# Kernel tuning notes

Hardware: AMD Instinct MI355X
Metric: run time of the kernel (lower is better)

## Reference

```python
import jax, jax.numpy as jnp
import numpy as np

NUM_EMBEDDINGS = 2048
EMBEDDING_DIM = 256
COMMITMENT_COST = 0.25


def setup_inputs() -> dict:
    key = jax.random.key(0)
    k1, k2 = jax.random.split(key)
    z_e = jax.random.normal(k1, (64, EMBEDDING_DIM, 32, 32), dtype=jnp.float32)
    # nn.Embedding weight initialized uniform(-1/K, 1/K)
    bound = 1.0 / NUM_EMBEDDINGS
    codebook = jax.random.uniform(k2, (NUM_EMBEDDINGS, EMBEDDING_DIM),
                                  dtype=jnp.float32, minval=-bound, maxval=bound)
    return {"z_e": z_e, "codebook": codebook}


def reference(z_e, codebook):
    B, C, H, W = z_e.shape  # C == embedding_dim
    K = codebook.shape[0]
    sg = jax.lax.stop_gradient

    # [B, C, H, W] -> [B*H*W, C]
    z_e_flat = jnp.transpose(z_e, (0, 2, 3, 1)).reshape(-1, C)

    # squared L2 distances: ||z||^2 - 2 z E^T + ||E||^2  -> [N, K]
    distances = (jnp.sum(z_e_flat ** 2, axis=1, keepdims=True)
                 - 2.0 * jnp.matmul(z_e_flat, codebook.T)
                 + jnp.sum(codebook ** 2, axis=1))
    indices = jnp.argmin(distances, axis=1)  # [N]

    encodings = jax.nn.one_hot(indices, K, dtype=z_e_flat.dtype)  # [N, K]
    z_q_flat = codebook[indices]  # [N, C] embedding gather
    z_q = jnp.transpose(z_q_flat.reshape(B, H, W, C), (0, 3, 1, 2))

    codebook_loss = jnp.mean((z_q_flat - sg(z_e_flat)) ** 2)
    commitment_loss = jnp.mean((sg(z_q_flat) - z_e_flat) ** 2)
    loss = codebook_loss + COMMITMENT_COST * commitment_loss

    e_mean = jnp.mean(encodings, axis=0)  # [K]
    perplexity = jnp.exp(-jnp.sum(e_mean * jnp.log(e_mean + 1e-10)))

    # straight-through estimator
    z_q_st = z_e + sg(z_q - z_e)
    return z_q_st, loss, perplexity, encodings
```

## Files before the change

### kernel.cpp

```cpp
#include <hip/hip_runtime.h>
#include <hip/hip_bf16.h>
#include <math.h>

#define NTOT 65536
#define KCB  2048
#define CDIM 256
#define HW   1024

#define OUT_LOSS 16777216
#define OUT_PERP 16777217
#define OUT_ENC  16777218

#define ZB_OFF_F  16777232
#define CBB_OFF_F 33554448

#define WS_SROW 0
#define WS_CK   262144
#define WS_IDX  270336
#define WS_CNT  532480
#define WS_PART 540672

#define MARGIN 3e-3f
#define CAP 4096

typedef __attribute__((ext_vector_type(8))) short short8;
typedef __attribute__((ext_vector_type(4))) float f32x4;

__device__ inline unsigned enc_f(float x) {
    unsigned u = __float_as_uint(x);
    return (u & 0x80000000u) ? ~u : (u | 0x80000000u);
}
__device__ inline float dec_f(unsigned e) {
    unsigned u = (e & 0x80000000u) ? (e ^ 0x80000000u) : ~e;
    return __uint_as_float(u);
}

__device__ inline void lds_min_u64(unsigned long long* p, unsigned long long v) {
    unsigned long long old = *p;
    while (v < old) {
        unsigned long long assumed = old;
        old = atomicCAS(p, assumed, v);
        if (old == assumed) break;
    }
}

__global__ __launch_bounds__(256) void k_prep_cb(const float* __restrict__ cb, ushort* __restrict__ cbb,
                                                 float* __restrict__ ck, int* __restrict__ cntK) {
    int wv = threadIdx.x >> 6, lane = threadIdx.x & 63;
    int r = blockIdx.x * 4 + wv;
    const float* row = cb + (size_t)r * CDIM;
    float4 v = *(const float4*)(row + lane * 4);
    ushort4 o;
    __hip_bfloat16 h;
    h = __float2bfloat16(v.x); o.x = *(ushort*)&h;
    h = __float2bfloat16(v.y); o.y = *(ushort*)&h;
    h = __float2bfloat16(v.z); o.z = *(ushort*)&h;
    h = __float2bfloat16(v.w); o.w = *(ushort*)&h;
    *(ushort4*)(cbb + (size_t)r * CDIM + lane * 4) = o;
    float s = v.x*v.x + v.y*v.y + v.z*v.z + v.w*v.w;
    for (int off = 32; off >= 1; off >>= 1) s += __shfl_down(s, off, 64);
    if (lane == 0) ck[r] = s;
    if (lane == 1) cntK[r] = 0;
}

__global__ __launch_bounds__(256) void k_rownorm(const float* __restrict__ z, float* __restrict__ srow) {
    int n = blockIdx.x * 256 + threadIdx.x;
    int b = n >> 10, hw = n & 1023;
    const float* base = z + (size_t)b * (CDIM * HW) + hw;
    float s = 0.f;
#pragma unroll 8
    for (int c = 0; c < CDIM; ++c) { float v = base[(size_t)c * HW]; s = fmaf(v, v, s); }
    srow[n] = s;
}

__global__ __launch_bounds__(256) void k_prep_z(const float* __restrict__ z, ushort* __restrict__ zb) {
    __shared__ float tile[64][65];
    int tid = threadIdx.x;
    int bid = blockIdx.x;
    int hwT = bid & 15, cT = (bid >> 4) & 3, b = bid >> 6;
    int c0 = cT * 64, hw0 = hwT * 64;
    int w = tid >> 6, hw = tid & 63;
#pragma unroll
    for (int l = 0; l < 16; ++l) {
        int c = l * 4 + w;
        tile[c][hw] = z[((size_t)b * CDIM + (c0 + c)) * HW + hw0 + hw];
    }
    __syncthreads();
    int r = tid >> 2, g = tid & 3;
    union { ushort u[16]; int4 v[2]; } pk;
#pragma unroll
    for (int j = 0; j < 16; ++j) {
        __hip_bfloat16 h = __float2bfloat16(tile[g * 16 + j][r]);
        pk.u[j] = *(ushort*)&h;
    }
    size_t n = (size_t)b * HW + hw0 + r;
    ushort* dst = zb + n * CDIM + c0 + g * 16;
    *(int4*)(dst) = pk.v[0];
    *(int4*)(dst + 8) = pk.v[1];
}

__global__ __launch_bounds__(256, 2) void k_mfma_argmin(
    const ushort* __restrict__ zb, const ushort* __restrict__ cbb,
    const float* __restrict__ z, const float* __restrict__ cb,
    const float* __restrict__ srow, const float* __restrict__ ckg,
    int* __restrict__ indices, int* __restrict__ cntK)
{
    __shared__ unsigned rowminU[64];
    __shared__ int   candRK[CAP];
    __shared__ float candD[CAP];
    __shared__ int   cnt;
    __shared__ float thrF[64];
    __shared__ unsigned long long best[64];

    const int tid = threadIdx.x;
    const int w = tid >> 6, lane = tid & 63;
    const int col = lane & 15, quad = lane >> 4;
    const int n0 = blockIdx.x * 64;

    short8 areg[4][8];
#pragma unroll
    for (int nt = 0; nt < 4; ++nt)
#pragma unroll
        for (int cs = 0; cs < 8; ++cs)
            areg[nt][cs] = *(const short8*)(zb + ((size_t)(n0 + nt * 16 + col)) * CDIM + cs * 32 + quad * 8);

    if (tid < 64) { rowminU[tid] = 0xFFFFFFFFu; best[tid] = ~0ull; }
    if (tid == 0) cnt = 0;

    float gmin[16];
#pragma unroll
    for (int s = 0; s < 16; ++s) gmin[s] = INFINITY;
    __syncthreads();

    int npass = 1;
    for (int pass = 0; pass < npass; ++pass) {
        for (int k0 = 0; k0 < KCB; k0 += 128) {
            const int kb = k0 + w * 32;
            f32x4 acc[4][2];
#pragma unroll
            for (int nt = 0; nt < 4; ++nt)
#pragma unroll
                for (int kt = 0; kt < 2; ++kt)
                    acc[nt][kt] = (f32x4){0.f, 0.f, 0.f, 0.f};
#pragma unroll
            for (int kt = 0; kt < 2; ++kt) {
                short8 bfrag[8];
#pragma unroll
                for (int cs = 0; cs < 8; ++cs)
                    bfrag[cs] = *(const short8*)(cbb + ((size_t)(kb + kt * 16 + col)) * CDIM + cs * 32 + quad * 8);
#pragma unroll
                for (int nt = 0; nt < 4; ++nt)
#pragma unroll
                    for (int cs = 0; cs < 8; ++cs)
                        acc[nt][kt] = __builtin_amdgcn_mfma_f32_16x16x32_bf16(areg[nt][cs], bfrag[cs], acc[nt][kt], 0, 0, 0);
            }
            if (pass == 0) {
#pragma unroll
                for (int kt = 0; kt < 2; ++kt) {
                    const float ckv = ckg[kb + kt * 16 + col];
#pragma unroll
                    for (int nt = 0; nt < 4; ++nt)
#pragma unroll
                        for (int r = 0; r < 4; ++r) {
                            float dt = fmaf(-2.0f, acc[nt][kt][r], ckv);
                            const int s = nt * 4 + r;
                            if (dt < gmin[s]) {
                                gmin[s] = dt;
                                atomicMin(&rowminU[nt * 16 + quad * 4 + r], enc_f(dt));
                            }
                        }
                }
            }
            __syncthreads();
#pragma unroll
            for (int s = 0; s < 16; ++s) {
                int row = (s >> 2) * 16 + quad * 4 + (s & 3);
                gmin[s] = fminf(gmin[s], dec_f(rowminU[row]));
            }
#pragma unroll
            for (int kt = 0; kt < 2; ++kt) {
                const int k = kb + kt * 16 + col;
                const float ckv = ckg[k];
#pragma unroll
                for (int nt = 0; nt < 4; ++nt)
#pragma unroll
                    for (int r = 0; r < 4; ++r) {
                        float dt = fmaf(-2.0f, acc[nt][kt][r], ckv);
                        const int s = nt * 4 + r;
                        if (dt <= gmin[s] + MARGIN) {
                            int p = atomicAdd(&cnt, 1);
                            if (p < CAP) {
                                candRK[p] = ((nt * 16 + quad * 4 + r) << 16) | k;
                                candD[p] = dt;
                            }
                        }
                    }
            }
        }
        __syncthreads();
        if (pass == 0 && cnt > CAP) {
            npass = 2;
            if (tid == 0) cnt = 0;
            __syncthreads();
        }
    }
    const int nc = min(cnt, CAP);
    if (tid < 64) thrF[tid] = dec_f(rowminU[tid]) + MARGIN;
    __syncthreads();

    const int b = n0 >> 10, hw0 = n0 & 1023;
    for (int t = tid; t < nc; t += 256) {
        const int rc = candRK[t];
        const int row = rc >> 16, k = rc & 0xFFFF;
        if (candD[t] > thrF[row]) continue;
        const float* zp = z + (size_t)b * (CDIM * HW) + hw0 + row;
        const float* cp = cb + (size_t)k * CDIM;
        float m = 0.f;
#pragma unroll 8
        for (int c = 0; c < CDIM; ++c) m = fmaf(zp[(size_t)c << 10], cp[c], m);
        float d = (srow[n0 + row] - 2.0f * m) + ckg[k];
        unsigned long long pk = ((unsigned long long)__float_as_uint(d) << 32) | (unsigned)k;
        lds_min_u64(&best[row], pk);
    }
    __syncthreads();
    if (tid < 64) {
        int bk = (int)(best[tid] & 0xFFFFFFFFull);
        indices[n0 + tid] = bk;
        atomicAdd(&cntK[bk], 1);
    }
}

__global__ __launch_bounds__(256, 2) void k_gather(const float* __restrict__ z, const float* __restrict__ cb,
                                                   const int* __restrict__ idx, float* __restrict__ out0,
                                                   double* __restrict__ part) {
    __shared__ float qt[CDIM * 64];
    __shared__ double sh[256];
    const int tid = threadIdx.x;
    const int nl = tid & 63, cg = tid >> 6;
    const int n0 = blockIdx.x * 64;
    const int b = n0 >> 10, hw0 = n0 & 1023;
    const int k = idx[n0 + nl];
    const float* crow = cb + (size_t)k * CDIM + cg * 64;
#pragma unroll
    for (int j4 = 0; j4 < 16; ++j4) {
        float4 v = *(const float4*)(crow + j4 * 4);
        int c = cg * 64 + j4 * 4;
        qt[(c + 0) * 64 + nl] = v.x;
        qt[(c + 1) * 64 + nl] = v.y;
        qt[(c + 2) * 64 + nl] = v.z;
        qt[(c + 3) * 64 + nl] = v.w;
    }
    __syncthreads();
    double acc = 0.0;
    const size_t ebase = ((size_t)b * CDIM) * HW + hw0 + nl;
#pragma unroll 4
    for (int j = 0; j < 64; ++j) {
        int c = cg * 64 + j;
        size_t e = ebase + ((size_t)c << 10);
        float ze = z[e];
        float q = qt[c * 64 + nl];
        float d = q - ze;
        out0[e] = ze + d;
        acc += (double)d * (double)d;
    }
    sh[tid] = acc;
    __syncthreads();
    for (int s = 128; s > 0; s >>= 1) {
        if (tid < s) sh[tid] += sh[tid + s];
        __syncthreads();
    }
    if (tid == 0) part[blockIdx.x] = sh[0];
}

__global__ __launch_bounds__(256) void k_encodings(const int* __restrict__ idx, float4* __restrict__ p4,
                                                   float* __restrict__ tail) {
    __shared__ int sidx[17];
    const int tid = threadIdx.x;
    const size_t g0 = (size_t)blockIdx.x * 8192;
    const long f0 = 4L * (long)g0 - 2;
    int nlo = (int)(f0 >> 11); if (nlo < 0) nlo = 0;
    if (tid < 17) { int n = nlo + tid; sidx[tid] = (n < NTOT) ? idx[n] : -1; }
    __syncthreads();
    const float4 zv = make_float4(0.f, 0.f, 0.f, 0.f);
    for (int i = 0; i < 32; ++i) {
        size_t g = g0 + (size_t)i * 256 + tid;
        long fe = 4L * (long)g - 2;
        float4 v = zv;
        if (fe < 0) {
            int kk = sidx[0];
            if (kk == 0) v.z = 1.f;
            if (kk == 1) v.w = 1.f;
        } else {
            int n = (int)(fe >> 11);
            int k0c = (int)(fe & 2047);
            if (k0c >= 2045) {
#pragma unroll
                for (int j = 0; j < 4; ++j) {
                    long fej = fe + j;
                    int nj = (int)(fej >> 11);
                    int kj = (int)(fej & 2047);
                    int li = nj - nlo;
                    int kk = (li >= 0 && li < 17) ? sidx[li] : -2;
                    ((float*)&v)[j] = (kk == kj) ? 1.f : 0.f;
                }
            } else {
                int d = sidx[n - nlo] - k0c;
                if (d >= 0 && d < 4) ((float*)&v)[d] = 1.f;
            }
        }
        p4[g] = v;
    }
    if (blockIdx.x == 0 && tid == 0) {
        int kk = idx[NTOT - 1];
        tail[0] = (kk == 2046) ? 1.f : 0.f;
        tail[1] = (kk == 2047) ? 1.f : 0.f;
    }
}

__global__ __launch_bounds__(256) void k_finalize(const double* __restrict__ part, const int* __restrict__ cnt,
                                                  float* __restrict__ out) {
    __shared__ double sh[256];
    double a = 0.0;
    for (int i = threadIdx.x; i < 1024; i += 256) a += part[i];
    sh[threadIdx.x] = a; __syncthreads();
    for (int s = 128; s > 0; s >>= 1) { if (threadIdx.x < s) sh[threadIdx.x] += sh[threadIdx.x + s]; __syncthreads(); }
    double total = sh[0];
    __syncthreads();
    double p = 0.0;
    for (int i = threadIdx.x; i < 2048; i += 256) {
        double pm = (double)cnt[i] / 65536.0;
        p += pm * log(pm + 1e-10);
    }
    sh[threadIdx.x] = p; __syncthreads();
    for (int s = 128; s > 0; s >>= 1) { if (threadIdx.x < s) sh[threadIdx.x] += sh[threadIdx.x + s]; __syncthreads(); }
    if (threadIdx.x == 0) {
        double mean = total / ((double)NTOT * (double)CDIM);
        out[OUT_LOSS] = (float)(mean * 1.25);
        out[OUT_PERP] = (float)exp(-sh[0]);
    }
}

extern "C" void kernel_launch(void* const* d_in, const int* in_sizes, int n_in,
                              void* d_out, int out_size, void* d_ws, size_t ws_size,
                              hipStream_t stream) {
    const float* z  = (const float*)d_in[0];
    const float* cb = (const float*)d_in[1];
    float* out = (float*)d_out;
    char* ws = (char*)d_ws;
    float*  srow = (float*)(ws + WS_SROW);
    float*  ck   = (float*)(ws + WS_CK);
    int*    idx  = (int*)(ws + WS_IDX);
    int*    cnt  = (int*)(ws + WS_CNT);
    double* part = (double*)(ws + WS_PART);
    ushort* zb  = (ushort*)(out + ZB_OFF_F);
    ushort* cbb = (ushort*)(out + CBB_OFF_F);

    hipLaunchKernelGGL(k_prep_cb,     dim3(512),  dim3(256), 0, stream, cb, cbb, ck, cnt);
    hipLaunchKernelGGL(k_rownorm,     dim3(256),  dim3(256), 0, stream, z, srow);
    hipLaunchKernelGGL(k_prep_z,      dim3(4096), dim3(256), 0, stream, z, zb);
    hipLaunchKernelGGL(k_mfma_argmin, dim3(1024), dim3(256), 0, stream, zb, cbb, z, cb, srow, ck, idx, cnt);
    hipLaunchKernelGGL(k_gather,      dim3(1024), dim3(256), 0, stream, z, cb, idx, out, part);
    hipLaunchKernelGGL(k_encodings,   dim3(4096), dim3(256), 0, stream, idx, (float4*)(out + OUT_LOSS),
                       out + (OUT_LOSS + (size_t)33554432 * 4));
    hipLaunchKernelGGL(k_finalize,    dim3(1),    dim3(256), 0, stream, part, cnt, out);
}
```

Measured before the change: 1.004 ms.

## Fuse prep kernels and restructure argmin with warm-start min and per-wave candidate lists

Merges the three preprocessing kernels into one launch with block-range dispatch. The argmin kernel now seeds the row minima from one codebook tile, then runs a single pass that updates minima and collects candidates together, with no per-tile block barrier. Candidates go into per-wave LDS lists of row/index only, so the candidate-distance array is gone. LDS drops enough to raise launch bounds to 3 blocks per CU. The trade-off is a looser candidate threshold early in the scan, which can mean more exact-refinement work, plus a full fallback rescan if any wave list overflows.

```diff
diff --git a/kernel.cpp b/kernel.cpp
--- a/kernel.cpp
+++ b/kernel.cpp
@@ -21,7 +21,7 @@
 #define WS_PART 540672
 
 #define MARGIN 3e-3f
-#define CAP 4096
+#define WCAP 1024
 
 typedef __attribute__((ext_vector_type(8))) short short8;
 typedef __attribute__((ext_vector_type(4))) float f32x4;
@@ -44,72 +44,92 @@
     }
 }
 
-__global__ __launch_bounds__(256) void k_prep_cb(const float* __restrict__ cb, ushort* __restrict__ cbb,
-                                                 float* __restrict__ ck, int* __restrict__ cntK) {
-    int wv = threadIdx.x >> 6, lane = threadIdx.x & 63;
-    int r = blockIdx.x * 4 + wv;
-    const float* row = cb + (size_t)r * CDIM;
-    float4 v = *(const float4*)(row + lane * 4);
-    ushort4 o;
-    __hip_bfloat16 h;
-    h = __float2bfloat16(v.x); o.x = *(ushort*)&h;
-    h = __float2bfloat16(v.y); o.y = *(ushort*)&h;
-    h = __float2bfloat16(v.z); o.z = *(ushort*)&h;
-    h = __float2bfloat16(v.w); o.w = *(ushort*)&h;
-    *(ushort4*)(cbb + (size_t)r * CDIM + lane * 4) = o;
-    float s = v.x*v.x + v.y*v.y + v.z*v.z + v.w*v.w;
-    for (int off = 32; off >= 1; off >>= 1) s += __shfl_down(s, off, 64);
-    if (lane == 0) ck[r] = s;
-    if (lane == 1) cntK[r] = 0;
-}
-
-__global__ __launch_bounds__(256) void k_rownorm(const float* __restrict__ z, float* __restrict__ srow) {
-    int n = blockIdx.x * 256 + threadIdx.x;
-    int b = n >> 10, hw = n & 1023;
-    const float* base = z + (size_t)b * (CDIM * HW) + hw;
-    float s = 0.f;
+__global__ __launch_bounds__(256) void k_prep(const float* __restrict__ z, const float* __restrict__ cb,
+                                              ushort* __restrict__ zb, ushort* __restrict__ cbb,
+                                              float* __restrict__ ck, float* __restrict__ srow,
+                                              int* __restrict__ cntK) {
+    __shared__ float tile[64][65];
+    const int tid = threadIdx.x;
+    const int bid = blockIdx.x;
+    if (bid < 512) {
+        int wv = tid >> 6, lane = tid & 63;
+        int r = bid * 4 + wv;
+        const float* row = cb + (size_t)r * CDIM;
+        float4 v = *(const float4*)(row + lane * 4);
+        ushort4 o;
+        __hip_bfloat16 h;
+        h = __float2bfloat16(v.x); o.x = *(ushort*)&h;
+        h = __float2bfloat16(v.y); o.y = *(ushort*)&h;
+        h = __float2bfloat16(v.z); o.z = *(ushort*)&h;
+        h = __float2bfloat16(v.w); o.w = *(ushort*)&h;
+        *(ushort4*)(cbb + (size_t)r * CDIM + lane * 4) = o;
+        float s = v.x*v.x + v.y*v.y + v.z*v.z + v.w*v.w;
+        for (int off = 32; off >= 1; off >>= 1) s += __shfl_down(s, off, 64);
+        if (lane == 0) ck[r] = s;
+        if (lane == 1) cntK[r] = 0;
+    } else if (bid < 768) {
+        int n = (bid - 512) * 256 + tid;
+        int b = n >> 10, hw = n & 1023;
+        const float* base = z + (size_t)b * (CDIM * HW) + hw;
+        float s = 0.f;
 #pragma unroll 8
-    for (int c = 0; c < CDIM; ++c) { float v = base[(size_t)c * HW]; s = fmaf(v, v, s); }
-    srow[n] = s;
-}
-
-__global__ __launch_bounds__(256) void k_prep_z(const float* __restrict__ z, ushort* __restrict__ zb) {
-    __shared__ float tile[64][65];
-    int tid = threadIdx.x;
-    int bid = blockIdx.x;
-    int hwT = bid & 15, cT = (bid >> 4) & 3, b = bid >> 6;
-    int c0 = cT * 64, hw0 = hwT * 64;
-    int w = tid >> 6, hw = tid & 63;
-#pragma unroll
-    for (int l = 0; l < 16; ++l) {
-        int c = l * 4 + w;
-        tile[c][hw] = z[((size_t)b * CDIM + (c0 + c)) * HW + hw0 + hw];
-    }
-    __syncthreads();
-    int r = tid >> 2, g = tid & 3;
-    union { ushort u[16]; int4 v[2]; } pk;
-#pragma unroll
-    for (int j = 0; j < 16; ++j) {
-        __hip_bfloat16 h = __float2bfloat16(tile[g * 16 + j][r]);
-        pk.u[j] = *(ushort*)&h;
-    }
-    size_t n = (size_t)b * HW + hw0 + r;
-    ushort* dst = zb + n * CDIM + c0 + g * 16;
-    *(int4*)(dst) = pk.v[0];
-    *(int4*)(dst + 8) = pk.v[1];
-}
-
-__global__ __launch_bounds__(256, 2) void k_mfma_argmin(
+        for (int c = 0; c < CDIM; ++c) { float v = base[(size_t)c * HW]; s = fmaf(v, v, s); }
+        srow[n] = s;
+    } else {
+        int zbid = bid - 768;
+        int hwT = zbid & 15, cT = (zbid >> 4) & 3, b = zbid >> 6;
+        int c0 = cT * 64, hw0 = hwT * 64;
+        int w = tid >> 6, hw = tid & 63;
+#pragma unroll
+        for (int l = 0; l < 16; ++l) {
+            int c = l * 4 + w;
+            tile[c][hw] = z[((size_t)b * CDIM + (c0 + c)) * HW + hw0 + hw];
+        }
+        __syncthreads();
+        int r = tid >> 2, g = tid & 3;
+        union { ushort u[16]; int4 v[2]; } pk;
+#pragma unroll
+        for (int j = 0; j < 16; ++j) {
+            __hip_bfloat16 h = __float2bfloat16(tile[g * 16 + j][r]);
+            pk.u[j] = *(ushort*)&h;
+        }
+        size_t n = (size_t)b * HW + hw0 + r;
+        ushort* dst = zb + n * CDIM + c0 + g * 16;
+        *(int4*)(dst) = pk.v[0];
+        *(int4*)(dst + 8) = pk.v[1];
+    }
+}
+
+__device__ __forceinline__ void tile_mfma(const ushort* __restrict__ cbb, int kb, int col, int quad,
+                                          const short8 (&areg)[4][8], f32x4 (&acc)[4][2]) {
+#pragma unroll
+    for (int nt = 0; nt < 4; ++nt)
+#pragma unroll
+        for (int kt = 0; kt < 2; ++kt)
+            acc[nt][kt] = (f32x4){0.f, 0.f, 0.f, 0.f};
+#pragma unroll
+    for (int kt = 0; kt < 2; ++kt) {
+        short8 bfrag[8];
+#pragma unroll
+        for (int cs = 0; cs < 8; ++cs)
+            bfrag[cs] = *(const short8*)(cbb + ((size_t)(kb + kt * 16 + col)) * CDIM + cs * 32 + quad * 8);
+#pragma unroll
+        for (int nt = 0; nt < 4; ++nt)
+#pragma unroll
+            for (int cs = 0; cs < 8; ++cs)
+                acc[nt][kt] = __builtin_amdgcn_mfma_f32_16x16x32_bf16(areg[nt][cs], bfrag[cs], acc[nt][kt], 0, 0, 0);
+    }
+}
+
+__global__ __launch_bounds__(256, 3) void k_mfma_argmin(
     const ushort* __restrict__ zb, const ushort* __restrict__ cbb,
     const float* __restrict__ z, const float* __restrict__ cb,
     const float* __restrict__ srow, const float* __restrict__ ckg,
     int* __restrict__ indices, int* __restrict__ cntK)
 {
     __shared__ unsigned rowminU[64];
-    __shared__ int   candRK[CAP];
-    __shared__ float candD[CAP];
-    __shared__ int   cnt;
-    __shared__ float thrF[64];
+    __shared__ int cand[4][WCAP];
+    __shared__ int wcnt[4];
     __shared__ unsigned long long best[64];
 
     const int tid = threadIdx.x;
@@ -125,58 +145,77 @@
             areg[nt][cs] = *(const short8*)(zb + ((size_t)(n0 + nt * 16 + col)) * CDIM + cs * 32 + quad * 8);
 
     if (tid < 64) { rowminU[tid] = 0xFFFFFFFFu; best[tid] = ~0ull; }
-    if (tid == 0) cnt = 0;
-
+    if (tid < 4) wcnt[tid] = 0;
     float gmin[16];
 #pragma unroll
     for (int s = 0; s < 16; ++s) gmin[s] = INFINITY;
     __syncthreads();
 
-    int npass = 1;
-    for (int pass = 0; pass < npass; ++pass) {
+    {
+        f32x4 acc[4][2];
+        tile_mfma(cbb, w * 32, col, quad, areg, acc);
+#pragma unroll
+        for (int kt = 0; kt < 2; ++kt) {
+            const float ckv = ckg[w * 32 + kt * 16 + col];
+#pragma unroll
+            for (int nt = 0; nt < 4; ++nt)
+#pragma unroll
+                for (int r = 0; r < 4; ++r) {
+                    float dt = fmaf(-2.0f, acc[nt][kt][r], ckv);
+                    const int s = nt * 4 + r;
+                    if (dt < gmin[s]) {
+                        gmin[s] = dt;
+                        atomicMin(&rowminU[nt * 16 + quad * 4 + r], enc_f(dt));
+                    }
+                }
+        }
+    }
+    __syncthreads();
+
+    for (int k0 = 0; k0 < KCB; k0 += 128) {
+        const int kb = k0 + w * 32;
+#pragma unroll
+        for (int s = 0; s < 16; ++s) {
+            int row = (s >> 2) * 16 + quad * 4 + (s & 3);
+            gmin[s] = fminf(gmin[s], dec_f(rowminU[row]));
+        }
+        f32x4 acc[4][2];
+        tile_mfma(cbb, kb, col, quad, areg, acc);
+#pragma unroll
+        for (int kt = 0; kt < 2; ++kt) {
+            const int k = kb + kt * 16 + col;
+            const float ckv = ckg[k];
+#pragma unroll
+            for (int nt = 0; nt < 4; ++nt)
+#pragma unroll
+                for (int r = 0; r < 4; ++r) {
+                    float dt = fmaf(-2.0f, acc[nt][kt][r], ckv);
+                    const int s = nt * 4 + r;
+                    const int row = nt * 16 + quad * 4 + r;
+                    if (dt < gmin[s]) {
+                        gmin[s] = dt;
+                        atomicMin(&rowminU[row], enc_f(dt));
+                    }
+                    if (dt <= gmin[s] + MARGIN) {
+                        int p = atomicAdd(&wcnt[w], 1);
+                        if (p < WCAP) cand[w][p] = (row << 16) | k;
+                    }
+                }
+        }
+    }
+    __syncthreads();
+
+    if (wcnt[0] > WCAP || wcnt[1] > WCAP || wcnt[2] > WCAP || wcnt[3] > WCAP) {
+        if (tid < 4) wcnt[tid] = 0;
+        __syncthreads();
+        float thr[16];
+#pragma unroll
+        for (int s = 0; s < 16; ++s)
+            thr[s] = dec_f(rowminU[(s >> 2) * 16 + quad * 4 + (s & 3)]) + MARGIN;
         for (int k0 = 0; k0 < KCB; k0 += 128) {
             const int kb = k0 + w * 32;
             f32x4 acc[4][2];
-#pragma unroll
-            for (int nt = 0; nt < 4; ++nt)
-#pragma unroll
-                for (int kt = 0; kt < 2; ++kt)
-                    acc[nt][kt] = (f32x4){0.f, 0.f, 0.f, 0.f};
-#pragma unroll
-            for (int kt = 0; kt < 2; ++kt) {
-                short8 bfrag[8];
-#pragma unroll
-                for (int cs = 0; cs < 8; ++cs)
-                    bfrag[cs] = *(const short8*)(cbb + ((size_t)(kb + kt * 16 + col)) * CDIM + cs * 32 + quad * 8);
-#pragma unroll
-                for (int nt = 0; nt < 4; ++nt)
-#pragma unroll
-                    for (int cs = 0; cs < 8; ++cs)
-                        acc[nt][kt] = __builtin_amdgcn_mfma_f32_16x16x32_bf16(areg[nt][cs], bfrag[cs], acc[nt][kt], 0, 0, 0);
-            }
-            if (pass == 0) {
-#pragma unroll
-                for (int kt = 0; kt < 2; ++kt) {
-                    const float ckv = ckg[kb + kt * 16 + col];
-#pragma unroll
-                    for (int nt = 0; nt < 4; ++nt)
-#pragma unroll
-                        for (int r = 0; r < 4; ++r) {
-                            float dt = fmaf(-2.0f, acc[nt][kt][r], ckv);
-                            const int s = nt * 4 + r;
-                            if (dt < gmin[s]) {
-                                gmin[s] = dt;
-                                atomicMin(&rowminU[nt * 16 + quad * 4 + r], enc_f(dt));
-                            }
-                        }
-                }
-            }
-            __syncthreads();
-#pragma unroll
-            for (int s = 0; s < 16; ++s) {
-                int row = (s >> 2) * 16 + quad * 4 + (s & 3);
-                gmin[s] = fminf(gmin[s], dec_f(rowminU[row]));
-            }
+            tile_mfma(cbb, kb, col, quad, areg, acc);
 #pragma unroll
             for (int kt = 0; kt < 2; ++kt) {
                 const int k = kb + kt * 16 + col;
@@ -186,41 +225,31 @@
 #pragma unroll
                     for (int r = 0; r < 4; ++r) {
                         float dt = fmaf(-2.0f, acc[nt][kt][r], ckv);
-                        const int s = nt * 4 + r;
-                        if (dt <= gmin[s] + MARGIN) {
-                            int p = atomicAdd(&cnt, 1);
-                            if (p < CAP) {
-                                candRK[p] = ((nt * 16 + quad * 4 + r) << 16) | k;
-                                candD[p] = dt;
-                            }
+                        if (dt <= thr[nt * 4 + r]) {
+                            int p = atomicAdd(&wcnt[w], 1);
+                            if (p < WCAP) cand[w][p] = ((nt * 16 + quad * 4 + r) << 16) | k;
                         }
                     }
             }
         }
         __syncthreads();
-        if (pass == 0 && cnt > CAP) {
-            npass = 2;
-            if (tid == 0) cnt = 0;
-            __syncthreads();
-        }
-    }
-    const int nc = min(cnt, CAP);
-    if (tid < 64) thrF[tid] = dec_f(rowminU[tid]) + MARGIN;
-    __syncthreads();
+    }
 
     const int b = n0 >> 10, hw0 = n0 & 1023;
-    for (int t = tid; t < nc; t += 256) {
-        const int rc = candRK[t];
-        const int row = rc >> 16, k = rc & 0xFFFF;
-        if (candD[t] > thrF[row]) continue;
-        const float* zp = z + (size_t)b * (CDIM * HW) + hw0 + row;
-        const float* cp = cb + (size_t)k * CDIM;
-        float m = 0.f;
+    for (int w2 = 0; w2 < 4; ++w2) {
+        const int nc = min(wcnt[w2], WCAP);
+        for (int t = tid; t < nc; t += 256) {
+            const int rc = cand[w2][t];
+            const int row = rc >> 16, k = rc & 0xFFFF;
+            const float* zp = z + (size_t)b * (CDIM * HW) + hw0 + row;
+            const float* cp = cb + (size_t)k * CDIM;
+            float m = 0.f;
 #pragma unroll 8
-        for (int c = 0; c < CDIM; ++c) m = fmaf(zp[(size_t)c << 10], cp[c], m);
-        float d = (srow[n0 + row] - 2.0f * m) + ckg[k];
-        unsigned long long pk = ((unsigned long long)__float_as_uint(d) << 32) | (unsigned)k;
-        lds_min_u64(&best[row], pk);
+            for (int c = 0; c < CDIM; ++c) m = fmaf(zp[(size_t)c << 10], cp[c], m);
+            float d = (srow[n0 + row] - 2.0f * m) + ckg[k];
+            unsigned long long pk = ((unsigned long long)__float_as_uint(d) << 32) | (unsigned)k;
+            lds_min_u64(&best[row], pk);
+        }
     }
     __syncthreads();
     if (tid < 64) {
@@ -355,9 +384,7 @@
     ushort* zb  = (ushort*)(out + ZB_OFF_F);
     ushort* cbb = (ushort*)(out + CBB_OFF_F);
 
-    hipLaunchKernelGGL(k_prep_cb,     dim3(512),  dim3(256), 0, stream, cb, cbb, ck, cnt);
-    hipLaunchKernelGGL(k_rownorm,     dim3(256),  dim3(256), 0, stream, z, srow);
-    hipLaunchKernelGGL(k_prep_z,      dim3(4096), dim3(256), 0, stream, z, zb);
+    hipLaunchKernelGGL(k_prep,        dim3(4864), dim3(256), 0, stream, z, cb, zb, cbb, ck, srow, cnt);
     hipLaunchKernelGGL(k_mfma_argmin, dim3(1024), dim3(256), 0, stream, zb, cbb, z, cb, srow, ck, idx, cnt);
     hipLaunchKernelGGL(k_gather,      dim3(1024), dim3(256), 0, stream, z, cb, idx, out, part);
     hipLaunchKernelGGL(k_encodings,   dim3(4096), dim3(256), 0, stream, idx, (float4*)(out + OUT_LOSS),
```

New measurement: 1.470 ms. 1.46x slower.
